# Optimization experiments

Hardware: AMD Instinct MI355X
Metric: run time of the kernel (lower is better)

Reference implementation:

```python
import jax, jax.numpy as jnp
import numpy as np

D_MODEL = 1024
STATE = 64
HEADS = 8
EXPAND = 2
INNER = EXPAND * D_MODEL          # 2048
HEAD_DIM = INNER // HEADS         # 256
PROJ_OUT = 2 * INNER + 2 * STATE + HEADS  # z, x, B, C, dt
BATCH, SEQ = 2, 1024
EPS = 1e-5


def setup_inputs() -> dict:
    key = jax.random.key(0)
    ks = jax.random.split(key, 6)
    g = lambda k, shape, sc: jax.random.normal(k, shape, jnp.float32) * sc
    return {
        "input_tensor": jax.random.normal(ks[0], (BATCH, SEQ, D_MODEL), jnp.float32),
        "ln_gamma": jnp.ones((D_MODEL,), jnp.float32),
        "ln_beta": jnp.zeros((D_MODEL,), jnp.float32),
        "W_in": g(ks[1], (D_MODEL, PROJ_OUT), 0.02),
        "b_in": jnp.zeros((PROJ_OUT,), jnp.float32),
        "A_log": jnp.log(jnp.arange(1, HEADS + 1, dtype=jnp.float32)),
        "D_skip": jnp.ones((HEADS,), jnp.float32),
        "dt_bias": g(ks[2], (HEADS,), 0.1),
        "W_out": g(ks[3], (INNER, D_MODEL), 0.02),
        "b_out": jnp.zeros((D_MODEL,), jnp.float32),
    }


def _layer_norm(x, gamma, beta):
    mu = jnp.mean(x, axis=-1, keepdims=True)
    xc = x - mu
    var = jnp.mean(xc * xc, axis=-1, keepdims=True)
    return xc * jax.lax.rsqrt(var + EPS) * gamma + beta


def _mamba2(u, W_in, b_in, A_log, D_skip, dt_bias, W_out, b_out):
    B, L, _ = u.shape
    zxbcdt = u @ W_in + b_in                                    # [B,L,PROJ_OUT]
    z = zxbcdt[..., :INNER]                                     # gate [B,L,INNER]
    xs = zxbcdt[..., INNER:2 * INNER].reshape(B, L, HEADS, HEAD_DIM)
    Bm = zxbcdt[..., 2 * INNER:2 * INNER + STATE]               # [B,L,N]
    Cm = zxbcdt[..., 2 * INNER + STATE:2 * INNER + 2 * STATE]   # [B,L,N]
    dt = jax.nn.softplus(zxbcdt[..., 2 * INNER + 2 * STATE:] + dt_bias)  # [B,L,H]

    A = -jnp.exp(A_log)                                         # [H], negative
    decay = jnp.exp(dt * A)                                     # [B,L,H]
    dtx = dt[..., None] * xs                                    # [B,L,H,P]

    # selective scan over time; state h: [B,H,P,N]
    def step(h, inp):
        dec_t, dtx_t, B_t, C_t = inp                            # [B,H],[B,H,P],[B,N],[B,N]
        h = dec_t[:, :, None, None] * h + dtx_t[..., None] * B_t[:, None, None, :]
        y = jnp.einsum('bhpn,bn->bhp', h, C_t)
        return h, y

    h0 = jnp.zeros((B, HEADS, HEAD_DIM, STATE), u.dtype)
    scan_in = (
        jnp.moveaxis(decay, 1, 0),   # [L,B,H]
        jnp.moveaxis(dtx, 1, 0),     # [L,B,H,P]
        jnp.moveaxis(Bm, 1, 0),      # [L,B,N]
        jnp.moveaxis(Cm, 1, 0),      # [L,B,N]
    )
    _, ys = jax.lax.scan(step, h0, scan_in)                     # [L,B,H,P]
    y = jnp.moveaxis(ys, 0, 1)                                  # [B,L,H,P]
    y = y + D_skip[None, None, :, None] * xs                    # skip connection
    y = y.reshape(B, L, INNER) * jax.nn.silu(z)                 # gated
    return y @ W_out + b_out


def reference(input_tensor, ln_gamma, ln_beta, W_in, b_in, A_log, D_skip, dt_bias, W_out, b_out):
    normed = _layer_norm(input_tensor, ln_gamma, ln_beta)
    out = _mamba2(normed, W_in, b_in, A_log, D_skip, dt_bias, W_out, b_out)
    return input_tensor + out
```

## Files before the change

### kernel.cpp

```cpp
#include <hip/hip_runtime.h>
#include <math.h>

#define D_MODEL 1024
#define STATE 64
#define HEADS 8
#define INNER 2048
#define HEAD_DIM 256
#define PROJ_OUT 4232
#define NPAD 4352
#define BATCH 2
#define SEQ 1024
#define NROWS (BATCH*SEQ)
#define EPS 1e-5f
#define BH (BATCH * HEADS)
#define LQ 64
#define NCH (SEQ / LQ)

typedef short s16x8 __attribute__((ext_vector_type(8)));
typedef float f32x4 __attribute__((ext_vector_type(4)));

#define LDS_AS(p) ((__attribute__((address_space(3))) void*)(p))
#define GLB_AS(p) ((const __attribute__((address_space(1))) void*)(p))

__device__ inline unsigned short f2bf(float f) {
    unsigned int u = __float_as_uint(f);
    unsigned int r = (u + 0x7fffu + ((u >> 16) & 1u)) >> 16;
    return (unsigned short)r;
}
__device__ inline float bf2f(unsigned short s) {
    return __uint_as_float(((unsigned int)s) << 16);
}
__device__ inline f32x4 mfma16(s16x8 a, s16x8 b, f32x4 c) {
    return __builtin_amdgcn_mfma_f32_16x16x32_bf16(a, b, c, 0, 0, 0);
}

__global__ __launch_bounds__(256) void ln_kernel(
    const float* __restrict__ x, const float* __restrict__ gamma,
    const float* __restrict__ beta, unsigned short* __restrict__ out)
{
    int row = blockIdx.x;
    int tid = threadIdx.x;
    const float4* xr = (const float4*)(x + (size_t)row * D_MODEL);
    float4 v = xr[tid];
    float s  = v.x + v.y + v.z + v.w;
    float sq = v.x*v.x + v.y*v.y + v.z*v.z + v.w*v.w;
    #pragma unroll
    for (int off = 32; off > 0; off >>= 1) {
        s  += __shfl_down(s,  off, 64);
        sq += __shfl_down(sq, off, 64);
    }
    __shared__ float ls[4], lq[4];
    int wave = tid >> 6, lane = tid & 63;
    if (lane == 0) { ls[wave] = s; lq[wave] = sq; }
    __syncthreads();
    s  = ls[0] + ls[1] + ls[2] + ls[3];
    sq = lq[0] + lq[1] + lq[2] + lq[3];
    float mu  = s * (1.f / D_MODEL);
    float var = sq * (1.f / D_MODEL) - mu * mu;
    float rs  = rsqrtf(var + EPS);
    float4 g  = ((const float4*)gamma)[tid];
    float4 bb = ((const float4*)beta)[tid];
    ushort4 o;
    o.x = f2bf((v.x - mu) * rs * g.x + bb.x);
    o.y = f2bf((v.y - mu) * rs * g.y + bb.y);
    o.z = f2bf((v.z - mu) * rs * g.z + bb.z);
    o.w = f2bf((v.w - mu) * rs * g.w + bb.w);
    ((ushort4*)(out + (size_t)row * D_MODEL))[tid] = o;
}

__global__ __launch_bounds__(256) void transpose_bf16(
    const float* __restrict__ in, unsigned short* __restrict__ out,
    int R, int C)
{
    __shared__ float tile[32][33];
    int c0 = blockIdx.x * 32;
    int r0 = blockIdx.y * 32;
    int tx = threadIdx.x & 31;
    int ty = threadIdx.x >> 5;
    #pragma unroll
    for (int i = 0; i < 4; ++i) {
        int r = ty + i * 8;
        int gc = c0 + tx;
        tile[r][tx] = (gc < C) ? in[(size_t)(r0 + r) * C + gc] : 0.f;
    }
    __syncthreads();
    #pragma unroll
    for (int i = 0; i < 4; ++i) {
        int oc = ty + i * 8;
        out[(size_t)(c0 + oc) * R + r0 + tx] = f2bf(tile[tx][oc]);
    }
}

template<int BM, int BN, bool HAS_ADD, bool GUARD_N>
__global__ __launch_bounds__(256) void gemm_bf16(
    const unsigned short* __restrict__ A, const unsigned short* __restrict__ BT,
    const float* __restrict__ bias, const float* __restrict__ add,
    float* __restrict__ C, int Nreal, int Nstride, int K)
{
    constexpr int FM = BM / 32;
    constexpr int FN = BN / 32;
    __shared__ unsigned short Asm[BM * 32];
    __shared__ unsigned short Bsm[BN * 32];
    const int tid = threadIdx.x;
    const int l = tid & 63, w = tid >> 6;
    const int lr = l & 15, lk = l >> 4;
    const int m0 = blockIdx.y * BM, n0 = blockIdx.x * BN;
    const int wm = w >> 1, wn = w & 1;

    f32x4 acc[FM][FN] = {};

    const unsigned short* Abase = A  + (size_t)(m0 + lr) * K + lk * 8;
    const unsigned short* Bbase = BT + (size_t)(n0 + lr) * K + lk * 8;

    for (int k0 = 0; k0 < K; k0 += 32) {
        #pragma unroll
        for (int i = 0; i < BM / 64; ++i) {
            int mb = w + 4 * i;
            __builtin_amdgcn_global_load_lds(
                GLB_AS(Abase + (size_t)mb * 16 * K + k0),
                LDS_AS(&Asm[mb * 512]), 16, 0, 0);
        }
        #pragma unroll
        for (int i = 0; i < BN / 64; ++i) {
            int nb = w + 4 * i;
            __builtin_amdgcn_global_load_lds(
                GLB_AS(Bbase + (size_t)nb * 16 * K + k0),
                LDS_AS(&Bsm[nb * 512]), 16, 0, 0);
        }
        __syncthreads();
        s16x8 af[FM], bfv[FN];
        #pragma unroll
        for (int i = 0; i < FM; ++i)
            af[i] = *(const s16x8*)&Asm[((wm * FM + i) * 64 + l) * 8];
        #pragma unroll
        for (int j = 0; j < FN; ++j)
            bfv[j] = *(const s16x8*)&Bsm[((wn * FN + j) * 64 + l) * 8];
        #pragma unroll
        for (int i = 0; i < FM; ++i)
            #pragma unroll
            for (int j = 0; j < FN; ++j)
                acc[i][j] = mfma16(af[i], bfv[j], acc[i][j]);
        __syncthreads();
    }

    #pragma unroll
    for (int i = 0; i < FM; ++i) {
        int row = m0 + (wm * FM + i) * 16 + lk * 4;
        #pragma unroll
        for (int j = 0; j < FN; ++j) {
            int col = n0 + (wn * FN + j) * 16 + lr;
            if (GUARD_N && col >= Nreal) continue;
            float bv = bias[col];
            #pragma unroll
            for (int r = 0; r < 4; ++r) {
                float v = acc[i][j][r] + bv;
                if (HAS_ADD) v += add[(size_t)(row + r) * Nstride + col];
                C[(size_t)(row + r) * Nstride + col] = v;
            }
        }
    }
}

__global__ __launch_bounds__(256) void ssd_pass1(
    const float* __restrict__ zx, const float* __restrict__ A_log,
    const float* __restrict__ dt_bias,
    unsigned short* __restrict__ Sbuf, float* __restrict__ Dk)
{
    __shared__ float w1s[LQ];
    __shared__ unsigned short xT[HEAD_DIM * LQ];
    __shared__ unsigned short BpT[STATE * LQ];
    int blk = blockIdx.x;
    int bh = blk >> 4, ck = blk & (NCH - 1);
    int b = bh >> 3, h = bh & 7;
    int tid = threadIdx.x;
    int l = tid & 63, w = tid >> 6;
    int lr = l & 15, lk = l >> 4;
    float a = -expf(A_log[h]);
    int t0 = ck * LQ;
    const float* zrow = zx + (size_t)(b * SEQ + t0) * PROJ_OUT;

    if (w == 0) {
        float dtr = zrow[(size_t)l * PROJ_OUT + 2 * INNER + 2 * STATE + h] + dt_bias[h];
        float dtv = (dtr > 20.f) ? dtr : log1pf(expf(dtr));
        float c = dtv;
        #pragma unroll
        for (int off = 1; off < 64; off <<= 1) {
            float v = __shfl_up(c, off, 64);
            if (l >= off) c += v;
        }
        float c63 = __shfl(c, 63, 64);
        w1s[l] = dtv * expf(a * (c63 - c));
        if (l == 63) Dk[bh * NCH + ck] = expf(a * c63);
    }
    {
        int p = tid;
        const float* xp = zrow + INNER + h * HEAD_DIM + p;
        int sw = (p & 7) << 3;
        #pragma unroll 4
        for (int tp = 0; tp < 32; ++tp) {
            float x0 = xp[(size_t)(2 * tp) * PROJ_OUT];
            float x1 = xp[(size_t)(2 * tp + 1) * PROJ_OUT];
            unsigned int pk = (unsigned int)f2bf(x0) | ((unsigned int)f2bf(x1) << 16);
            *(unsigned int*)&xT[p * LQ + ((2 * tp) ^ sw)] = pk;
        }
    }
    __syncthreads();
    #pragma unroll
    for (int i = 0; i < 16; ++i) {
        int e = i * 256 + tid;
        int t = e >> 6, n = e & 63;
        float v = zrow[(size_t)t * PROJ_OUT + 2 * INNER + n] * w1s[t];
        BpT[n * LQ + (t ^ ((n & 7) << 3))] = f2bf(v);
    }
    __syncthreads();

    f32x4 acc[4][4] = {};
    #pragma unroll
    for (int kk = 0; kk < 2; ++kk) {
        int krun = kk * 32 + lk * 8;
        s16x8 bfr[4];
        #pragma unroll
        for (int j = 0; j < 4; ++j) {
            int n = j * 16 + lr;
            bfr[j] = *(const s16x8*)&BpT[n * LQ + (krun ^ ((n & 7) << 3))];
        }
        #pragma unroll
        for (int i = 0; i < 4; ++i) {
            int p = (w * 4 + i) * 16 + lr;
            s16x8 afr = *(const s16x8*)&xT[p * LQ + (krun ^ ((p & 7) << 3))];
            #pragma unroll
            for (int j = 0; j < 4; ++j)
                acc[i][j] = mfma16(afr, bfr[j], acc[i][j]);
        }
    }
    unsigned short* sp = Sbuf + ((size_t)bh * NCH + ck) * (STATE * HEAD_DIM);
    #pragma unroll
    for (int i = 0; i < 4; ++i) {
        int p = (w * 4 + i) * 16 + lk * 4;
        #pragma unroll
        for (int j = 0; j < 4; ++j) {
            int n = j * 16 + lr;
            #pragma unroll
            for (int r = 0; r < 4; ++r)
                sp[(size_t)(p + r) * STATE + n] = f2bf(acc[i][j][r]);
        }
    }
}

template<int NCHq>
__global__ __launch_bounds__(256) void scan_combine(
    unsigned short* __restrict__ Sbuf, const float* __restrict__ Dk)
{
    int bh = blockIdx.y;
    int e  = blockIdx.x * 256 + threadIdx.x;
    size_t base = (size_t)bh * NCHq * (STATE * HEAD_DIM) + e;
    float h = 0.f;
    #pragma unroll
    for (int k = 0; k < NCHq; ++k) {
        size_t idx = base + (size_t)k * (STATE * HEAD_DIM);
        float s = bf2f(Sbuf[idx]);
        Sbuf[idx] = f2bf(h);
        h = Dk[bh * NCHq + k] * h + s;
    }
}

__global__ __launch_bounds__(256) void ssd_pass2(
    const float* __restrict__ zx, const float* __restrict__ A_log,
    const float* __restrict__ D_skip, const float* __restrict__ dt_bias,
    const unsigned short* __restrict__ Sbuf, unsigned short* __restrict__ yg)
{
    __shared__ float dts[LQ], cums[LQ];
    __shared__ unsigned short xT[HEAD_DIM * LQ];
    __shared__ unsigned short Cm[LQ * STATE];
    __shared__ unsigned short Cd[LQ * STATE];
    __shared__ unsigned short Bm[LQ * STATE];
    __shared__ unsigned short Pp[LQ * LQ];
    int blk = blockIdx.x;
    int bh = blk >> 4, ck = blk & (NCH - 1);
    int b = bh >> 3, h = bh & 7;
    int tid = threadIdx.x;
    int l = tid & 63, w = tid >> 6;
    int lr = l & 15, lk = l >> 4;
    float a = -expf(A_log[h]);
    float dsk = D_skip[h];
    int t0 = ck * LQ;
    const float* zrow = zx + (size_t)(b * SEQ + t0) * PROJ_OUT;

    if (w == 0) {
        float dtr = zrow[(size_t)l * PROJ_OUT + 2 * INNER + 2 * STATE + h] + dt_bias[h];
        float dtv = (dtr > 20.f) ? dtr : log1pf(expf(dtr));
        float c = dtv;
        #pragma unroll
        for (int off = 1; off < 64; off <<= 1) {
            float v = __shfl_up(c, off, 64);
            if (l >= off) c += v;
        }
        dts[l] = dtv;
        cums[l] = c;
    }
    {
        int p = tid;
        const float* xp = zrow + INNER + h * HEAD_DIM + p;
        int sw = (p & 7) << 3;
        #pragma unroll 4
        for (int tp = 0; tp < 32; ++tp) {
            float x0 = xp[(size_t)(2 * tp) * PROJ_OUT];
            float x1 = xp[(size_t)(2 * tp + 1) * PROJ_OUT];
            unsigned int pk = (unsigned int)f2bf(x0) | ((unsigned int)f2bf(x1) << 16);
            *(unsigned int*)&xT[p * LQ + ((2 * tp) ^ sw)] = pk;
        }
    }
    __syncthreads();
    #pragma unroll
    for (int i = 0; i < 16; ++i) {
        int e = i * 256 + tid;
        int t = e >> 6, n = e & 63;
        int sn = n ^ ((t & 7) << 3);
        float cv = zrow[(size_t)t * PROJ_OUT + 2 * INNER + STATE + n];
        float bv = zrow[(size_t)t * PROJ_OUT + 2 * INNER + n];
        Cm[t * STATE + sn] = f2bf(cv);
        Cd[t * STATE + sn] = f2bf(cv * expf(a * cums[t]));
        Bm[t * STATE + sn] = f2bf(bv);
    }
    __syncthreads();

    const unsigned short* hbase = Sbuf + ((size_t)bh * NCH + ck) * (STATE * HEAD_DIM);
    s16x8 h0f[4][2];
    #pragma unroll
    for (int j = 0; j < 4; ++j) {
        int p = w * 64 + j * 16 + lr;
        #pragma unroll
        for (int kk = 0; kk < 2; ++kk)
            h0f[j][kk] = *(const s16x8*)&hbase[(size_t)p * STATE + kk * 32 + lk * 8];
    }

    f32x4 pa[4] = {};
    #pragma unroll
    for (int kk = 0; kk < 2; ++kk) {
        int krun = kk * 32 + lk * 8;
        int tA = w * 16 + lr;
        s16x8 afr = *(const s16x8*)&Cm[tA * STATE + (krun ^ ((tA & 7) << 3))];
        #pragma unroll
        for (int j = 0; j < 4; ++j) {
            int sB = j * 16 + lr;
            s16x8 bfr = *(const s16x8*)&Bm[sB * STATE + (krun ^ ((sB & 7) << 3))];
            pa[j] = mfma16(afr, bfr, pa[j]);
        }
    }
    #pragma unroll
    for (int j = 0; j < 4; ++j) {
        #pragma unroll
        for (int r = 0; r < 4; ++r) {
            int t = w * 16 + lk * 4 + r;
            int s = j * 16 + lr;
            float sc = (s <= t) ? dts[s] * expf(a * (cums[t] - cums[s])) : 0.f;
            Pp[t * LQ + (s ^ ((t & 7) << 3))] = f2bf(pa[j][r] * sc);
        }
    }
    __syncthreads();

    f32x4 ya[4][4] = {};
    #pragma unroll
    for (int kk = 0; kk < 2; ++kk) {
        int krun = kk * 32 + lk * 8;
        s16x8 bfr[4];
        #pragma unroll
        for (int j = 0; j < 4; ++j) {
            int p = w * 64 + j * 16 + lr;
            bfr[j] = *(const s16x8*)&xT[p * LQ + (krun ^ ((p & 7) << 3))];
        }
        #pragma unroll
        for (int i = 0; i < 4; ++i) {
            int t = i * 16 + lr;
            s16x8 afr = *(const s16x8*)&Pp[t * LQ + (krun ^ ((t & 7) << 3))];
            #pragma unroll
            for (int j = 0; j < 4; ++j)
                ya[i][j] = mfma16(afr, bfr[j], ya[i][j]);
        }
    }
    #pragma unroll
    for (int kk = 0; kk < 2; ++kk) {
        int krun = kk * 32 + lk * 8;
        #pragma unroll
        for (int i = 0; i < 4; ++i) {
            int t = i * 16 + lr;
            s16x8 afr = *(const s16x8*)&Cd[t * STATE + (krun ^ ((t & 7) << 3))];
            #pragma unroll
            for (int j = 0; j < 4; ++j)
                ya[i][j] = mfma16(afr, h0f[j][kk], ya[i][j]);
        }
    }

    #pragma unroll
    for (int i = 0; i < 4; ++i) {
        #pragma unroll
        for (int r = 0; r < 4; ++r) {
            int t = i * 16 + lk * 4 + r;
            #pragma unroll
            for (int j = 0; j < 4; ++j) {
                int p = w * 64 + j * 16 + lr;
                float xv = bf2f(xT[p * LQ + (t ^ ((p & 7) << 3))]);
                float z = zrow[(size_t)t * PROJ_OUT + h * HEAD_DIM + p];
                float y = ya[i][j][r] + dsk * xv;
                float gate = z / (1.f + expf(-z));
                yg[(size_t)(b * SEQ + t0 + t) * INNER + h * HEAD_DIM + p] = f2bf(y * gate);
            }
        }
    }
}

__global__ __launch_bounds__(256) void scan_serial(
    const float* __restrict__ zx,
    const float* __restrict__ A_log, const float* __restrict__ D_skip,
    const float* __restrict__ dt_bias,
    unsigned short* __restrict__ yg)
{
    int bh = blockIdx.x;
    int b  = bh >> 3, h = bh & 7;
    int p  = threadIdx.x;
    float a   = -expf(A_log[h]);
    float dsk = D_skip[h];
    float dtb = dt_bias[h];

    float hs[STATE];
    #pragma unroll
    for (int n = 0; n < STATE; ++n) hs[n] = 0.f;

    for (int t = 0; t < SEQ; ++t) {
        const float* row = zx + (size_t)(b * SEQ + t) * PROJ_OUT;
        float dtr = row[2 * INNER + 2 * STATE + h] + dtb;
        float dt  = (dtr > 20.f) ? dtr : log1pf(expf(dtr));
        float dec = expf(dt * a);
        float x   = row[INNER + h * HEAD_DIM + p];
        float z   = row[h * HEAD_DIM + p];
        float dtx = dt * x;
        #pragma unroll
        for (int n = 0; n < STATE; ++n)
            hs[n] = dec * hs[n] + dtx * row[2 * INNER + n];
        float y0 = 0.f, y1 = 0.f, y2 = 0.f, y3 = 0.f;
        #pragma unroll
        for (int n = 0; n < STATE; n += 4) {
            y0 += hs[n + 0] * row[2 * INNER + STATE + n + 0];
            y1 += hs[n + 1] * row[2 * INNER + STATE + n + 1];
            y2 += hs[n + 2] * row[2 * INNER + STATE + n + 2];
            y3 += hs[n + 3] * row[2 * INNER + STATE + n + 3];
        }
        float y = (y0 + y1) + (y2 + y3) + dsk * x;
        float gate = z / (1.f + expf(-z));
        yg[(size_t)(b * SEQ + t) * INNER + h * HEAD_DIM + p] = f2bf(y * gate);
    }
}

extern "C" void kernel_launch(void* const* d_in, const int* in_sizes, int n_in,
                              void* d_out, int out_size, void* d_ws, size_t ws_size,
                              hipStream_t stream) {
    const float* input  = (const float*)d_in[0];
    const float* gamma  = (const float*)d_in[1];
    const float* beta   = (const float*)d_in[2];
    const float* W_in   = (const float*)d_in[3];
    const float* b_in   = (const float*)d_in[4];
    const float* A_log  = (const float*)d_in[5];
    const float* D_skip = (const float*)d_in[6];
    const float* dt_b   = (const float*)d_in[7];
    const float* W_out  = (const float*)d_in[8];
    const float* b_out  = (const float*)d_in[9];
    float* out = (float*)d_out;

    char* ws = (char*)d_ws;
    size_t off = 0;
    unsigned short* normed_bf = (unsigned short*)(ws + off); off += (size_t)NROWS * D_MODEL * 2;
    float*          zx        = (float*)(ws + off);          off += (size_t)NROWS * PROJ_OUT * 4;
    unsigned short* yg        = (unsigned short*)(ws + off); off += (size_t)NROWS * INNER * 2;
    unsigned short* WT        = (unsigned short*)(ws + off); off += (size_t)NPAD * D_MODEL * 2;
    unsigned short* WoT       = (unsigned short*)(ws + off); off += (size_t)D_MODEL * INNER * 2;
    unsigned short* Sbuf      = (unsigned short*)(ws + off); off += (size_t)BH * NCH * STATE * HEAD_DIM * 2;
    off = (off + 255) & ~(size_t)255;
    float*          Dk        = (float*)(ws + off);          off += (size_t)BH * NCH * 4;
    bool ssd = (off <= ws_size);

    dim3 gt1(NPAD / 32, D_MODEL / 32);
    transpose_bf16<<<gt1, 256, 0, stream>>>(W_in, WT, D_MODEL, PROJ_OUT);
    dim3 gt2(D_MODEL / 32, INNER / 32);
    transpose_bf16<<<gt2, 256, 0, stream>>>(W_out, WoT, INNER, D_MODEL);

    ln_kernel<<<NROWS, 256, 0, stream>>>(input, gamma, beta, normed_bf);

    dim3 g1(NPAD / 128, NROWS / 128);
    gemm_bf16<128, 128, false, true><<<g1, 256, 0, stream>>>(
        normed_bf, WT, b_in, nullptr, zx, PROJ_OUT, PROJ_OUT, D_MODEL);

    if (ssd) {
        ssd_pass1<<<BH * NCH, 256, 0, stream>>>(zx, A_log, dt_b, Sbuf, Dk);
        dim3 gc(STATE * HEAD_DIM / 256, BH);
        scan_combine<NCH><<<gc, 256, 0, stream>>>(Sbuf, Dk);
        ssd_pass2<<<BH * NCH, 256, 0, stream>>>(zx, A_log, D_skip, dt_b, Sbuf, yg);
    } else {
        scan_serial<<<BH, 256, 0, stream>>>(zx, A_log, D_skip, dt_b, yg);
    }

    dim3 g2(D_MODEL / 64, NROWS / 64);
    gemm_bf16<64, 64, true, false><<<g2, 256, 0, stream>>>(
        yg, WoT, b_out, input, out, D_MODEL, D_MODEL, INNER);
}
```

Baseline: 138.2 us.

## Store in-projection output as bf16 with fp32 dt side buffer and halve SSD chunk length

The input projection GEMM now writes its output as bf16 instead of fp32, plus a separate fp32 buffer for the dt columns so the softplus/cumsum inputs keep full precision. This halves the bytes written by the big GEMM and read by the SSD passes. The chunk length drops from 64 to 32, which doubles the number of SSD blocks and halves per-block intra-chunk work; pass2's matmul tiling is restructured to match. The cost is more chunks for the sequential combine step and bf16 rounding of z, x, B and C before the scan.

```diff
diff --git a/kernel.cpp b/kernel.cpp
--- a/kernel.cpp
+++ b/kernel.cpp
@@ -7,13 +7,14 @@
 #define INNER 2048
 #define HEAD_DIM 256
 #define PROJ_OUT 4232
+#define DT_OFF  4224
 #define NPAD 4352
 #define BATCH 2
 #define SEQ 1024
 #define NROWS (BATCH*SEQ)
 #define EPS 1e-5f
 #define BH (BATCH * HEADS)
-#define LQ 64
+#define LQ 32
 #define NCH (SEQ / LQ)
 
 typedef short s16x8 __attribute__((ext_vector_type(8)));
@@ -91,11 +92,12 @@
     }
 }
 
-template<int BM, int BN, bool HAS_ADD, bool GUARD_N>
+template<int BM, int BN, bool HAS_ADD, bool GUARD_N, bool OUT_BF16>
 __global__ __launch_bounds__(256) void gemm_bf16(
     const unsigned short* __restrict__ A, const unsigned short* __restrict__ BT,
     const float* __restrict__ bias, const float* __restrict__ add,
-    float* __restrict__ C, int Nreal, int Nstride, int K)
+    float* __restrict__ C, unsigned short* __restrict__ Cb,
+    float* __restrict__ dtb, int Nreal, int Nstride, int K)
 {
     constexpr int FM = BM / 32;
     constexpr int FN = BN / 32;
@@ -155,79 +157,86 @@
             for (int r = 0; r < 4; ++r) {
                 float v = acc[i][j][r] + bv;
                 if (HAS_ADD) v += add[(size_t)(row + r) * Nstride + col];
-                C[(size_t)(row + r) * Nstride + col] = v;
+                if (OUT_BF16) {
+                    Cb[(size_t)(row + r) * Nstride + col] = f2bf(v);
+                    if (col >= DT_OFF)
+                        dtb[(size_t)(row + r) * HEADS + (col - DT_OFF)] = v;
+                } else {
+                    C[(size_t)(row + r) * Nstride + col] = v;
+                }
             }
         }
     }
 }
 
 __global__ __launch_bounds__(256) void ssd_pass1(
-    const float* __restrict__ zx, const float* __restrict__ A_log,
-    const float* __restrict__ dt_bias,
+    const unsigned short* __restrict__ zx, const float* __restrict__ dtbuf,
+    const float* __restrict__ A_log, const float* __restrict__ dt_bias,
     unsigned short* __restrict__ Sbuf, float* __restrict__ Dk)
 {
     __shared__ float w1s[LQ];
     __shared__ unsigned short xT[HEAD_DIM * LQ];
     __shared__ unsigned short BpT[STATE * LQ];
     int blk = blockIdx.x;
-    int bh = blk >> 4, ck = blk & (NCH - 1);
+    int bh = blk >> 5, ck = blk & (NCH - 1);
     int b = bh >> 3, h = bh & 7;
     int tid = threadIdx.x;
     int l = tid & 63, w = tid >> 6;
     int lr = l & 15, lk = l >> 4;
     float a = -expf(A_log[h]);
     int t0 = ck * LQ;
-    const float* zrow = zx + (size_t)(b * SEQ + t0) * PROJ_OUT;
+    const unsigned short* zrow = zx + (size_t)(b * SEQ + t0) * PROJ_OUT;
 
     if (w == 0) {
-        float dtr = zrow[(size_t)l * PROJ_OUT + 2 * INNER + 2 * STATE + h] + dt_bias[h];
+        int tl = l & 31;
+        float dtr = dtbuf[(size_t)(b * SEQ + t0 + tl) * HEADS + h] + dt_bias[h];
         float dtv = (dtr > 20.f) ? dtr : log1pf(expf(dtr));
         float c = dtv;
         #pragma unroll
-        for (int off = 1; off < 64; off <<= 1) {
+        for (int off = 1; off < 32; off <<= 1) {
             float v = __shfl_up(c, off, 64);
-            if (l >= off) c += v;
-        }
-        float c63 = __shfl(c, 63, 64);
-        w1s[l] = dtv * expf(a * (c63 - c));
-        if (l == 63) Dk[bh * NCH + ck] = expf(a * c63);
+            if ((l & 31) >= off) c += v;
+        }
+        float c31 = __shfl(c, 31, 64);
+        if (l < 32) {
+            w1s[l] = dtv * expf(a * (c31 - c));
+            if (l == 31) Dk[bh * NCH + ck] = expf(a * c31);
+        }
     }
     {
         int p = tid;
-        const float* xp = zrow + INNER + h * HEAD_DIM + p;
-        int sw = (p & 7) << 3;
-        #pragma unroll 4
-        for (int tp = 0; tp < 32; ++tp) {
-            float x0 = xp[(size_t)(2 * tp) * PROJ_OUT];
-            float x1 = xp[(size_t)(2 * tp + 1) * PROJ_OUT];
-            unsigned int pk = (unsigned int)f2bf(x0) | ((unsigned int)f2bf(x1) << 16);
-            *(unsigned int*)&xT[p * LQ + ((2 * tp) ^ sw)] = pk;
-        }
-    }
-    __syncthreads();
-    #pragma unroll
-    for (int i = 0; i < 16; ++i) {
+        const unsigned short* xp = zrow + INNER + h * HEAD_DIM + p;
+        int sw = (p & 3) << 3;
+        #pragma unroll
+        for (int tp = 0; tp < 16; ++tp) {
+            unsigned int x0 = xp[(size_t)(2 * tp) * PROJ_OUT];
+            unsigned int x1 = xp[(size_t)(2 * tp + 1) * PROJ_OUT];
+            *(unsigned int*)&xT[p * LQ + ((2 * tp) ^ sw)] = x0 | (x1 << 16);
+        }
+    }
+    __syncthreads();
+    #pragma unroll
+    for (int i = 0; i < 8; ++i) {
         int e = i * 256 + tid;
         int t = e >> 6, n = e & 63;
-        float v = zrow[(size_t)t * PROJ_OUT + 2 * INNER + n] * w1s[t];
-        BpT[n * LQ + (t ^ ((n & 7) << 3))] = f2bf(v);
+        float v = bf2f(zrow[(size_t)t * PROJ_OUT + 2 * INNER + n]) * w1s[t];
+        BpT[n * LQ + (t ^ ((n & 3) << 3))] = f2bf(v);
     }
     __syncthreads();
 
     f32x4 acc[4][4] = {};
-    #pragma unroll
-    for (int kk = 0; kk < 2; ++kk) {
-        int krun = kk * 32 + lk * 8;
+    {
+        int krun = lk * 8;
         s16x8 bfr[4];
         #pragma unroll
         for (int j = 0; j < 4; ++j) {
             int n = j * 16 + lr;
-            bfr[j] = *(const s16x8*)&BpT[n * LQ + (krun ^ ((n & 7) << 3))];
+            bfr[j] = *(const s16x8*)&BpT[n * LQ + (krun ^ ((n & 3) << 3))];
         }
         #pragma unroll
         for (int i = 0; i < 4; ++i) {
             int p = (w * 4 + i) * 16 + lr;
-            s16x8 afr = *(const s16x8*)&xT[p * LQ + (krun ^ ((p & 7) << 3))];
+            s16x8 afr = *(const s16x8*)&xT[p * LQ + (krun ^ ((p & 3) << 3))];
             #pragma unroll
             for (int j = 0; j < 4; ++j)
                 acc[i][j] = mfma16(afr, bfr[j], acc[i][j]);
@@ -255,7 +264,7 @@
     int e  = blockIdx.x * 256 + threadIdx.x;
     size_t base = (size_t)bh * NCHq * (STATE * HEAD_DIM) + e;
     float h = 0.f;
-    #pragma unroll
+    #pragma unroll 8
     for (int k = 0; k < NCHq; ++k) {
         size_t idx = base + (size_t)k * (STATE * HEAD_DIM);
         float s = bf2f(Sbuf[idx]);
@@ -265,8 +274,9 @@
 }
 
 __global__ __launch_bounds__(256) void ssd_pass2(
-    const float* __restrict__ zx, const float* __restrict__ A_log,
-    const float* __restrict__ D_skip, const float* __restrict__ dt_bias,
+    const unsigned short* __restrict__ zx, const float* __restrict__ dtbuf,
+    const float* __restrict__ A_log, const float* __restrict__ D_skip,
+    const float* __restrict__ dt_bias,
     const unsigned short* __restrict__ Sbuf, unsigned short* __restrict__ yg)
 {
     __shared__ float dts[LQ], cums[LQ];
@@ -276,7 +286,7 @@
     __shared__ unsigned short Bm[LQ * STATE];
     __shared__ unsigned short Pp[LQ * LQ];
     int blk = blockIdx.x;
-    int bh = blk >> 4, ck = blk & (NCH - 1);
+    int bh = blk >> 5, ck = blk & (NCH - 1);
     int b = bh >> 3, h = bh & 7;
     int tid = threadIdx.x;
     int l = tid & 63, w = tid >> 6;
@@ -284,43 +294,41 @@
     float a = -expf(A_log[h]);
     float dsk = D_skip[h];
     int t0 = ck * LQ;
-    const float* zrow = zx + (size_t)(b * SEQ + t0) * PROJ_OUT;
+    const unsigned short* zrow = zx + (size_t)(b * SEQ + t0) * PROJ_OUT;
 
     if (w == 0) {
-        float dtr = zrow[(size_t)l * PROJ_OUT + 2 * INNER + 2 * STATE + h] + dt_bias[h];
+        int tl = l & 31;
+        float dtr = dtbuf[(size_t)(b * SEQ + t0 + tl) * HEADS + h] + dt_bias[h];
         float dtv = (dtr > 20.f) ? dtr : log1pf(expf(dtr));
         float c = dtv;
         #pragma unroll
-        for (int off = 1; off < 64; off <<= 1) {
+        for (int off = 1; off < 32; off <<= 1) {
             float v = __shfl_up(c, off, 64);
-            if (l >= off) c += v;
-        }
-        dts[l] = dtv;
-        cums[l] = c;
+            if ((l & 31) >= off) c += v;
+        }
+        if (l < 32) { dts[l] = dtv; cums[l] = c; }
     }
     {
         int p = tid;
-        const float* xp = zrow + INNER + h * HEAD_DIM + p;
-        int sw = (p & 7) << 3;
-        #pragma unroll 4
-        for (int tp = 0; tp < 32; ++tp) {
-            float x0 = xp[(size_t)(2 * tp) * PROJ_OUT];
-            float x1 = xp[(size_t)(2 * tp + 1) * PROJ_OUT];
-            unsigned int pk = (unsigned int)f2bf(x0) | ((unsigned int)f2bf(x1) << 16);
-            *(unsigned int*)&xT[p * LQ + ((2 * tp) ^ sw)] = pk;
-        }
-    }
-    __syncthreads();
-    #pragma unroll
-    for (int i = 0; i < 16; ++i) {
+        const unsigned short* xp = zrow + INNER + h * HEAD_DIM + p;
+        int sw = (p & 3) << 3;
+        #pragma unroll
+        for (int tp = 0; tp < 16; ++tp) {
+            unsigned int x0 = xp[(size_t)(2 * tp) * PROJ_OUT];
+            unsigned int x1 = xp[(size_t)(2 * tp + 1) * PROJ_OUT];
+            *(unsigned int*)&xT[p * LQ + ((2 * tp) ^ sw)] = x0 | (x1 << 16);
+        }
+    }
+    __syncthreads();
+    #pragma unroll
+    for (int i = 0; i < 8; ++i) {
         int e = i * 256 + tid;
         int t = e >> 6, n = e & 63;
         int sn = n ^ ((t & 7) << 3);
-        float cv = zrow[(size_t)t * PROJ_OUT + 2 * INNER + STATE + n];
-        float bv = zrow[(size_t)t * PROJ_OUT + 2 * INNER + n];
-        Cm[t * STATE + sn] = f2bf(cv);
-        Cd[t * STATE + sn] = f2bf(cv * expf(a * cums[t]));
-        Bm[t * STATE + sn] = f2bf(bv);
+        unsigned short cv = zrow[(size_t)t * PROJ_OUT + 2 * INNER + STATE + n];
+        Cm[t * STATE + sn] = cv;
+        Cd[t * STATE + sn] = f2bf(bf2f(cv) * expf(a * cums[t]));
+        Bm[t * STATE + sn] = zrow[(size_t)t * PROJ_OUT + 2 * INNER + n];
     }
     __syncthreads();
 
@@ -334,55 +342,48 @@
             h0f[j][kk] = *(const s16x8*)&hbase[(size_t)p * STATE + kk * 32 + lk * 8];
     }
 
-    f32x4 pa[4] = {};
+    f32x4 pa = {};
     #pragma unroll
     for (int kk = 0; kk < 2; ++kk) {
         int krun = kk * 32 + lk * 8;
-        int tA = w * 16 + lr;
+        int tA = (w >> 1) * 16 + lr;
+        int sB = (w & 1) * 16 + lr;
         s16x8 afr = *(const s16x8*)&Cm[tA * STATE + (krun ^ ((tA & 7) << 3))];
+        s16x8 bfr = *(const s16x8*)&Bm[sB * STATE + (krun ^ ((sB & 7) << 3))];
+        pa = mfma16(afr, bfr, pa);
+    }
+    #pragma unroll
+    for (int r = 0; r < 4; ++r) {
+        int t = (w >> 1) * 16 + lk * 4 + r;
+        int s = (w & 1) * 16 + lr;
+        float sc = (s <= t) ? dts[s] * expf(a * (cums[t] - cums[s])) : 0.f;
+        Pp[t * LQ + (s ^ ((t & 3) << 3))] = f2bf(pa[r] * sc);
+    }
+    __syncthreads();
+
+    f32x4 ya[2][4] = {};
+    {
+        int krun = lk * 8;
+        s16x8 bfr[4];
         #pragma unroll
         for (int j = 0; j < 4; ++j) {
-            int sB = j * 16 + lr;
-            s16x8 bfr = *(const s16x8*)&Bm[sB * STATE + (krun ^ ((sB & 7) << 3))];
-            pa[j] = mfma16(afr, bfr, pa[j]);
-        }
-    }
-    #pragma unroll
-    for (int j = 0; j < 4; ++j) {
-        #pragma unroll
-        for (int r = 0; r < 4; ++r) {
-            int t = w * 16 + lk * 4 + r;
-            int s = j * 16 + lr;
-            float sc = (s <= t) ? dts[s] * expf(a * (cums[t] - cums[s])) : 0.f;
-            Pp[t * LQ + (s ^ ((t & 7) << 3))] = f2bf(pa[j][r] * sc);
-        }
-    }
-    __syncthreads();
-
-    f32x4 ya[4][4] = {};
+            int p = w * 64 + j * 16 + lr;
+            bfr[j] = *(const s16x8*)&xT[p * LQ + (krun ^ ((p & 3) << 3))];
+        }
+        #pragma unroll
+        for (int i = 0; i < 2; ++i) {
+            int t = i * 16 + lr;
+            s16x8 afr = *(const s16x8*)&Pp[t * LQ + (krun ^ ((t & 3) << 3))];
+            #pragma unroll
+            for (int j = 0; j < 4; ++j)
+                ya[i][j] = mfma16(afr, bfr[j], ya[i][j]);
+        }
+    }
     #pragma unroll
     for (int kk = 0; kk < 2; ++kk) {
         int krun = kk * 32 + lk * 8;
-        s16x8 bfr[4];
-        #pragma unroll
-        for (int j = 0; j < 4; ++j) {
-            int p = w * 64 + j * 16 + lr;
-            bfr[j] = *(const s16x8*)&xT[p * LQ + (krun ^ ((p & 7) << 3))];
-        }
-        #pragma unroll
-        for (int i = 0; i < 4; ++i) {
-            int t = i * 16 + lr;
-            s16x8 afr = *(const s16x8*)&Pp[t * LQ + (krun ^ ((t & 7) << 3))];
-            #pragma unroll
-            for (int j = 0; j < 4; ++j)
-                ya[i][j] = mfma16(afr, bfr[j], ya[i][j]);
-        }
-    }
-    #pragma unroll
-    for (int kk = 0; kk < 2; ++kk) {
-        int krun = kk * 32 + lk * 8;
-        #pragma unroll
-        for (int i = 0; i < 4; ++i) {
+        #pragma unroll
+        for (int i = 0; i < 2; ++i) {
             int t = i * 16 + lr;
             s16x8 afr = *(const s16x8*)&Cd[t * STATE + (krun ^ ((t & 7) << 3))];
             #pragma unroll
@@ -392,15 +393,15 @@
     }
 
     #pragma unroll
-    for (int i = 0; i < 4; ++i) {
+    for (int i = 0; i < 2; ++i) {
         #pragma unroll
         for (int r = 0; r < 4; ++r) {
             int t = i * 16 + lk * 4 + r;
             #pragma unroll
             for (int j = 0; j < 4; ++j) {
                 int p = w * 64 + j * 16 + lr;
-                float xv = bf2f(xT[p * LQ + (t ^ ((p & 7) << 3))]);
-                float z = zrow[(size_t)t * PROJ_OUT + h * HEAD_DIM + p];
+                float xv = bf2f(xT[p * LQ + (t ^ ((p & 3) << 3))]);
+                float z  = bf2f(zrow[(size_t)t * PROJ_OUT + h * HEAD_DIM + p]);
                 float y = ya[i][j][r] + dsk * xv;
                 float gate = z / (1.f + expf(-z));
                 yg[(size_t)(b * SEQ + t0 + t) * INNER + h * HEAD_DIM + p] = f2bf(y * gate);
@@ -410,7 +411,7 @@
 }
 
 __global__ __launch_bounds__(256) void scan_serial(
-    const float* __restrict__ zx,
+    const unsigned short* __restrict__ zx, const float* __restrict__ dtbuf,
     const float* __restrict__ A_log, const float* __restrict__ D_skip,
     const float* __restrict__ dt_bias,
     unsigned short* __restrict__ yg)
@@ -427,25 +428,21 @@
     for (int n = 0; n < STATE; ++n) hs[n] = 0.f;
 
     for (int t = 0; t < SEQ; ++t) {
-        const float* row = zx + (size_t)(b * SEQ + t) * PROJ_OUT;
-        float dtr = row[2 * INNER + 2 * STATE + h] + dtb;
+        const unsigned short* row = zx + (size_t)(b * SEQ + t) * PROJ_OUT;
+        float dtr = dtbuf[(size_t)(b * SEQ + t) * HEADS + h] + dtb;
         float dt  = (dtr > 20.f) ? dtr : log1pf(expf(dtr));
         float dec = expf(dt * a);
-        float x   = row[INNER + h * HEAD_DIM + p];
-        float z   = row[h * HEAD_DIM + p];
+        float x   = bf2f(row[INNER + h * HEAD_DIM + p]);
+        float z   = bf2f(row[h * HEAD_DIM + p]);
         float dtx = dt * x;
         #pragma unroll
         for (int n = 0; n < STATE; ++n)
-            hs[n] = dec * hs[n] + dtx * row[2 * INNER + n];
-        float y0 = 0.f, y1 = 0.f, y2 = 0.f, y3 = 0.f;
-        #pragma unroll
-        for (int n = 0; n < STATE; n += 4) {
-            y0 += hs[n + 0] * row[2 * INNER + STATE + n + 0];
-            y1 += hs[n + 1] * row[2 * INNER + STATE + n + 1];
-            y2 += hs[n + 2] * row[2 * INNER + STATE + n + 2];
-            y3 += hs[n + 3] * row[2 * INNER + STATE + n + 3];
-        }
-        float y = (y0 + y1) + (y2 + y3) + dsk * x;
+            hs[n] = dec * hs[n] + dtx * bf2f(row[2 * INNER + n]);
+        float y0 = 0.f;
+        #pragma unroll
+        for (int n = 0; n < STATE; ++n)
+            y0 += hs[n] * bf2f(row[2 * INNER + STATE + n]);
+        float y = y0 + dsk * x;
         float gate = z / (1.f + expf(-z));
         yg[(size_t)(b * SEQ + t) * INNER + h * HEAD_DIM + p] = f2bf(y * gate);
     }
@@ -469,7 +466,8 @@
     char* ws = (char*)d_ws;
     size_t off = 0;
     unsigned short* normed_bf = (unsigned short*)(ws + off); off += (size_t)NROWS * D_MODEL * 2;
-    float*          zx        = (float*)(ws + off);          off += (size_t)NROWS * PROJ_OUT * 4;
+    unsigned short* zx        = (unsigned short*)(ws + off); off += (size_t)NROWS * PROJ_OUT * 2;
+    float*          dtbuf     = (float*)(ws + off);          off += (size_t)NROWS * HEADS * 4;
     unsigned short* yg        = (unsigned short*)(ws + off); off += (size_t)NROWS * INNER * 2;
     unsigned short* WT        = (unsigned short*)(ws + off); off += (size_t)NPAD * D_MODEL * 2;
     unsigned short* WoT       = (unsigned short*)(ws + off); off += (size_t)D_MODEL * INNER * 2;
@@ -486,19 +484,19 @@
     ln_kernel<<<NROWS, 256, 0, stream>>>(input, gamma, beta, normed_bf);
 
     dim3 g1(NPAD / 128, NROWS / 128);
-    gemm_bf16<128, 128, false, true><<<g1, 256, 0, stream>>>(
-        normed_bf, WT, b_in, nullptr, zx, PROJ_OUT, PROJ_OUT, D_MODEL);
+    gemm_bf16<128, 128, false, true, true><<<g1, 256, 0, stream>>>(
+        normed_bf, WT, b_in, nullptr, nullptr, zx, dtbuf, PROJ_OUT, PROJ_OUT, D_MODEL);
 
     if (ssd) {
-        ssd_pass1<<<BH * NCH, 256, 0, stream>>>(zx, A_log, dt_b, Sbuf, Dk);
+        ssd_pass1<<<BH * NCH, 256, 0, stream>>>(zx, dtbuf, A_log, dt_b, Sbuf, Dk);
         dim3 gc(STATE * HEAD_DIM / 256, BH);
         scan_combine<NCH><<<gc, 256, 0, stream>>>(Sbuf, Dk);
-        ssd_pass2<<<BH * NCH, 256, 0, stream>>>(zx, A_log, D_skip, dt_b, Sbuf, yg);
+        ssd_pass2<<<BH * NCH, 256, 0, stream>>>(zx, dtbuf, A_log, D_skip, dt_b, Sbuf, yg);
     } else {
-        scan_serial<<<BH, 256, 0, stream>>>(zx, A_log, D_skip, dt_b, yg);
+        scan_serial<<<BH, 256, 0, stream>>>(zx, dtbuf, A_log, D_skip, dt_b, yg);
     }
 
     dim3 g2(D_MODEL / 64, NROWS / 64);
-    gemm_bf16<64, 64, true, false><<<g2, 256, 0, stream>>>(
-        yg, WoT, b_out, input, out, D_MODEL, D_MODEL, INNER);
-}
+    gemm_bf16<64, 64, true, false, false><<<g2, 256, 0, stream>>>(
+        yg, WoT, b_out, input, out, nullptr, nullptr, D_MODEL, D_MODEL, INNER);
+}
```

New measurement: 135.4 us. 1.02x faster.
